# Optimization experiments

Measured on AMD Instinct MI355X. Metric: run time of the kernel, lower is better.

## Reference

```python
import jax, jax.numpy as jnp
import numpy as np

B, C, N, T = 16, 32, 1024, 64
C_OUT = 32
ORDER = 2
SMOOTH_DEPTH = 1


def setup_inputs() -> dict:
    key = jax.random.key(0)
    k1, k2, k3, k4 = jax.random.split(key, 4)
    x = jax.random.normal(k1, (B, C, N, T), dtype=jnp.float32)
    # row-normalized dense adjacencies (transition matrices), as used in Graph-WaveNet-style supports
    AL = jax.random.uniform(k2, (N, N), dtype=jnp.float32)
    AL = AL / AL.sum(axis=-1, keepdims=True)
    AS_pos = jax.random.uniform(k3, (N, N), dtype=jnp.float32)
    AS_pos = AS_pos / AS_pos.sum(axis=-1, keepdims=True)
    # 1x1 conv mlp: in_channels = (order*support_len+1)*c_in = 3*C, out_channels = C_OUT
    W_mlp = jax.random.normal(k4, (C_OUT, (ORDER + 1) * C), dtype=jnp.float32) * 0.02
    b_mlp = jnp.zeros((C_OUT,), dtype=jnp.float32)
    return {"x": x, "AL": AL, "AS_pos": AS_pos, "W_mlp": W_mlp, "b_mlp": b_mlp}


def reference(x, AL, AS_pos, W_mlp, b_mlp):
    # gcn_module.forward with short_bool=True, smooth_depth=SMOOTH_DEPTH, eval mode (no dropout)
    ALp = jnp.linalg.matrix_power(AL, SMOOTH_DEPTH)          # [N,N]
    # torch.einsum('bckj,ik->bcij', x, ALp): contract node dim of x against ALp
    x_long = jnp.einsum('ik,bckt->bcit', ALp, x)             # [B,C,N,T]
    x_short = x - x_long
    outs = [x]
    for _ in range(ORDER):
        # dnconv: einsum('nvw,ncwl->ncvl', A, x) with 2D A broadcast over batch
        x_long = jnp.einsum('vw,bcwt->bcvt', AL, x_long)
        x_short = jnp.einsum('vw,bcwt->bcvt', AS_pos, x_short)
        outs.append(x_long + x_short)
    h = jnp.concatenate(outs, axis=1)                        # [B,(ORDER+1)*C,N,T]
    # 1x1 conv == channel mixing
    h = jnp.einsum('oc,bcnt->bont', W_mlp, h) + b_mlp[None, :, None, None]
    return h
```

## Files before the change

### kernel.cpp

```cpp
#include <hip/hip_runtime.h>


typedef __bf16 bf16x8 __attribute__((ext_vector_type(8)));
typedef float f32x4 __attribute__((ext_vector_type(4)));
typedef unsigned int u32x4 __attribute__((ext_vector_type(4)));
typedef unsigned int u32x2 __attribute__((ext_vector_type(2)));

__device__ __forceinline__ unsigned short f2bf(float f) {
  unsigned u = __builtin_bit_cast(unsigned, f);
  u += 0x7fffu + ((u >> 16) & 1u);
  return (unsigned short)(u >> 16);
}
__device__ __forceinline__ float bf2f(unsigned short h) {
  unsigned u = ((unsigned)h) << 16;
  return __builtin_bit_cast(float, u);
}

static constexpr size_t OFF_XT    = 0;
static constexpr size_t OFF_U     = 67108864;
static constexpr size_t OFF_ALBF  = 201326592;
static constexpr size_t OFF_ALT   = OFF_ALBF  + 2097152;
static constexpr size_t OFF_ASBF  = OFF_ALT   + 2097152;
static constexpr size_t OFF_AST   = OFF_ASBF  + 2097152;
static constexpr size_t OFF_AL2   = OFF_AST   + 2097152;
static constexpr size_t OFF_AL2T  = OFF_AL2   + 2097152;
static constexpr size_t OFF_ASAL  = OFF_AL2T  + 2097152;
static constexpr size_t OFF_AS2   = OFF_ASAL  + 2097152;
static constexpr size_t OFF_AL3   = OFF_AS2   + 2097152;
static constexpr size_t OFF_AS2AL = OFF_AL3   + 2097152;
static constexpr size_t OFF_G     = OFF_AS2AL + 2097152;

__global__ __launch_bounds__(256) void k_cast_bf16(const float* __restrict__ src,
                                                   unsigned short* __restrict__ dst,
                                                   int n4) {
  int i = blockIdx.x * 256 + threadIdx.x;
  if (i < n4) {
    float4 v = *((const float4*)src + i);
    unsigned lo = (unsigned)f2bf(v.x) | ((unsigned)f2bf(v.y) << 16);
    unsigned hi = (unsigned)f2bf(v.z) | ((unsigned)f2bf(v.w) << 16);
    u32x2 pk = {lo, hi};
    *(u32x2*)(dst + (size_t)i * 4) = pk;
  }
}

__global__ __launch_bounds__(256) void k_transpose_cast(const float* __restrict__ src,
                                                        unsigned short* __restrict__ dst,
                                                        int R, int Cc) {
  __shared__ float Xs[64][65];
  const int tid = threadIdx.x;
  const size_t slice = (size_t)blockIdx.z * (size_t)R * (size_t)Cc;
  const float* s = src + slice;
  unsigned short* d = dst + slice;
  const int r0 = blockIdx.x * 64, c0 = blockIdx.y * 64;
  const int lrow = tid >> 4, lc4 = tid & 15;
#pragma unroll
  for (int rr = 0; rr < 4; rr++) {
    int row = rr * 16 + lrow;
    float4 v = *(const float4*)(s + (size_t)(r0 + row) * Cc + c0 + lc4 * 4);
    Xs[row][lc4 * 4 + 0] = v.x;
    Xs[row][lc4 * 4 + 1] = v.y;
    Xs[row][lc4 * 4 + 2] = v.z;
    Xs[row][lc4 * 4 + 3] = v.w;
  }
  __syncthreads();
  const int wc = tid & 7;
#pragma unroll
  for (int u = 0; u < 2; u++) {
    int t = u * 32 + (tid >> 3);
    unsigned v0 = (unsigned)f2bf(Xs[wc * 8 + 0][t]) | ((unsigned)f2bf(Xs[wc * 8 + 1][t]) << 16);
    unsigned v1 = (unsigned)f2bf(Xs[wc * 8 + 2][t]) | ((unsigned)f2bf(Xs[wc * 8 + 3][t]) << 16);
    unsigned v2 = (unsigned)f2bf(Xs[wc * 8 + 4][t]) | ((unsigned)f2bf(Xs[wc * 8 + 5][t]) << 16);
    unsigned v3 = (unsigned)f2bf(Xs[wc * 8 + 6][t]) | ((unsigned)f2bf(Xs[wc * 8 + 7][t]) << 16);
    u32x4 pk = {v0, v1, v2, v3};
    *(u32x4*)(d + (size_t)(c0 + t) * R + r0 + wc * 8) = pk;
  }
}

__device__ __forceinline__ void gemm128_bt(const unsigned short* __restrict__ A,
                                           const unsigned short* __restrict__ Bt,
                                           unsigned short* __restrict__ Cp,
                                           int K, size_t ldc, int m0, int n0) {
  __shared__ unsigned short As[128 * 32];
  __shared__ unsigned short Bs[128 * 32];
  const int tid = threadIdx.x;
  const int wave = tid >> 6, lane = tid & 63;
  const int lane15 = lane & 15, quad = lane >> 4;
  const int wm = wave & 1, wn = wave >> 1;
  const int srow = lane >> 2;
  const int schunk = (lane & 3) * 8;

  const unsigned short* gA0 = A + (size_t)(m0 + wave * 16 + srow) * K + schunk;
  const unsigned short* gA1 = A + (size_t)(m0 + 64 + wave * 16 + srow) * K + schunk;
  const unsigned short* gB0 = Bt + (size_t)(n0 + wave * 16 + srow) * K + schunk;
  const unsigned short* gB1 = Bt + (size_t)(n0 + 64 + wave * 16 + srow) * K + schunk;
  unsigned short* lA0 = As + (wave * 16) * 32;
  unsigned short* lA1 = As + (64 + wave * 16) * 32;
  unsigned short* lB0 = Bs + (wave * 16) * 32;
  unsigned short* lB1 = Bs + (64 + wave * 16) * 32;

  f32x4 acc[4][4];
#pragma unroll
  for (int i = 0; i < 4; i++)
#pragma unroll
    for (int j = 0; j < 4; j++) acc[i][j] = (f32x4){0.f, 0.f, 0.f, 0.f};

  const unsigned short* pa = As + (wm * 64 + lane15) * 32 + quad * 8;
  const unsigned short* pb = Bs + (wn * 64 + lane15) * 32 + quad * 8;

  for (int kb = 0; kb < K; kb += 32) {
    __syncthreads();
    __builtin_amdgcn_global_load_lds(
        (const __attribute__((address_space(1))) unsigned int*)(gA0 + kb),
        (__attribute__((address_space(3))) unsigned int*)lA0, 16, 0, 0);
    __builtin_amdgcn_global_load_lds(
        (const __attribute__((address_space(1))) unsigned int*)(gA1 + kb),
        (__attribute__((address_space(3))) unsigned int*)lA1, 16, 0, 0);
    __builtin_amdgcn_global_load_lds(
        (const __attribute__((address_space(1))) unsigned int*)(gB0 + kb),
        (__attribute__((address_space(3))) unsigned int*)lB0, 16, 0, 0);
    __builtin_amdgcn_global_load_lds(
        (const __attribute__((address_space(1))) unsigned int*)(gB1 + kb),
        (__attribute__((address_space(3))) unsigned int*)lB1, 16, 0, 0);
    __syncthreads();

    bf16x8 av[4], bv[4];
#pragma unroll
    for (int mt = 0; mt < 4; mt++) av[mt] = *(const bf16x8*)(pa + mt * 16 * 32);
#pragma unroll
    for (int nt = 0; nt < 4; nt++) bv[nt] = *(const bf16x8*)(pb + nt * 16 * 32);
#pragma unroll
    for (int mt = 0; mt < 4; mt++)
#pragma unroll
      for (int nt = 0; nt < 4; nt++)
        acc[mt][nt] = __builtin_amdgcn_mfma_f32_16x16x32_bf16(av[mt], bv[nt], acc[mt][nt], 0, 0, 0);
  }

#pragma unroll
  for (int mt = 0; mt < 4; mt++) {
#pragma unroll
    for (int nt = 0; nt < 4; nt++) {
      const int col = n0 + wn * 64 + nt * 16 + lane15;
#pragma unroll
      for (int r = 0; r < 4; r++) {
        const int row = m0 + wm * 64 + mt * 16 + quad * 4 + r;
        Cp[(size_t)row * ldc + col] = f2bf(acc[mt][nt][r]);
      }
    }
  }
}

__global__ __launch_bounds__(256) void k_gemm_pre(char* ws, int stage) {
  const unsigned short* A;
  const unsigned short* Bt;
  unsigned short* Cp;
  const int z = blockIdx.z;
  unsigned short* ALbf = (unsigned short*)(ws + OFF_ALBF);
  unsigned short* ALt  = (unsigned short*)(ws + OFF_ALT);
  unsigned short* ASbf = (unsigned short*)(ws + OFF_ASBF);
  unsigned short* ASt  = (unsigned short*)(ws + OFF_AST);
  unsigned short* AL2  = (unsigned short*)(ws + OFF_AL2);
  unsigned short* AL2t = (unsigned short*)(ws + OFF_AL2T);
  unsigned short* ASAL = (unsigned short*)(ws + OFF_ASAL);
  unsigned short* AS2  = (unsigned short*)(ws + OFF_AS2);
  unsigned short* AL3  = (unsigned short*)(ws + OFF_AL3);
  unsigned short* AS2AL= (unsigned short*)(ws + OFF_AS2AL);
  if (stage == 0) {
    if (z == 0)      { A = ALbf; Bt = ALt;  Cp = AL2;  }
    else if (z == 1) { A = ALt;  Bt = ALbf; Cp = AL2t; }
    else if (z == 2) { A = ASbf; Bt = ALt;  Cp = ASAL; }
    else             { A = ASbf; Bt = ASt;  Cp = AS2;  }
  } else {
    if (z == 0)      { A = ALbf; Bt = AL2t; Cp = AL3;  }
    else             { A = AS2;  Bt = ALt;  Cp = AS2AL;}
  }
  gemm128_bt(A, Bt, Cp, 1024, 1024, blockIdx.y * 128, blockIdx.x * 128);
}

__global__ __launch_bounds__(256) void k_assemble_G(const unsigned short* __restrict__ AL2,
                                                    const unsigned short* __restrict__ ASAL,
                                                    const float* __restrict__ ASf,
                                                    const unsigned short* __restrict__ AL3,
                                                    const unsigned short* __restrict__ AS2,
                                                    const unsigned short* __restrict__ AS2AL,
                                                    unsigned short* __restrict__ G) {
  int i = blockIdx.x * 256 + threadIdx.x;
  float g1 = bf2f(AL2[i]) + ASf[i] - bf2f(ASAL[i]);
  G[i] = f2bf(g1);
  float g2 = bf2f(AL3[i]) + bf2f(AS2[i]) - bf2f(AS2AL[i]);
  G[1048576 + i] = f2bf(g2);
}

__global__ __launch_bounds__(256) void k_gemm_main(const unsigned short* __restrict__ G,
                                                   const unsigned short* __restrict__ xT,
                                                   unsigned short* __restrict__ U) {
  gemm128_bt(G, xT, U, 1024, 32768, blockIdx.y * 128, blockIdx.x * 128);
}

__device__ __forceinline__ int swz_off(int j, int kc) {
  int s = (j ^ (j >> 3) ^ (j >> 6)) & 7;
  return (kc ^ s) << 3;
}

__global__ __launch_bounds__(256) void k_mix_mfma(const float* __restrict__ x,
                                                  const unsigned short* __restrict__ U,
                                                  const unsigned short* __restrict__ Wbf,
                                                  const float* __restrict__ bm,
                                                  float* __restrict__ out) {
  __shared__ unsigned short Hs[128 * 128];
  const int tid = threadIdx.x;
  const int b  = blockIdx.x >> 9;
  const int n0 = (blockIdx.x & 511) * 2;

  const float* xb = x + (size_t)b * 2097152 + (size_t)n0 * 64;
#pragma unroll
  for (int i = 0; i < 4; i++) {
    int q = tid + 256 * i;
    int p = q >> 4;
    int c = p >> 1, nn = p & 1;
    int t0 = (q & 15) * 4;
    float4 v = *(const float4*)(xb + (size_t)c * 65536 + nn * 64 + t0);
    int kc = c >> 3, wi = c & 7;
    float vv[4] = {v.x, v.y, v.z, v.w};
#pragma unroll
    for (int e = 0; e < 4; e++) {
      int j = nn * 64 + t0 + e;
      Hs[j * 128 + swz_off(j, kc) + wi] = f2bf(vv[e]);
    }
  }
#pragma unroll
  for (int i = 0; i < 4; i++) {
    int q = tid + 256 * i;
    int row = q >> 8;
    int g = row >> 1, nn = row & 1;
    int s8 = (q & 255) * 8;
    int c = s8 >> 6, t0 = s8 & 63;
    const unsigned short* src =
        U + (size_t)(g * 1024 + n0 + nn) * 32768 + (size_t)b * 2048 + s8;
    u32x4 v = *(const u32x4*)src;
    int kc = 4 + g * 4 + (c >> 3), wi = c & 7;
#pragma unroll
    for (int e = 0; e < 4; e++) {
      int j0 = nn * 64 + t0 + 2 * e;
      unsigned w = v[e];
      Hs[j0 * 128 + swz_off(j0, kc) + wi]       = (unsigned short)(w & 0xffffu);
      Hs[(j0 + 1) * 128 + swz_off(j0 + 1, kc) + wi] = (unsigned short)(w >> 16);
    }
  }
  __syncthreads();

  const int wave = tid >> 6, lane = tid & 63;
  const int lane15 = lane & 15, quad = lane >> 4;
  f32x4 acc[2][2];
#pragma unroll
  for (int jt = 0; jt < 2; jt++)
#pragma unroll
    for (int ot = 0; ot < 2; ot++) acc[jt][ot] = (f32x4){0.f, 0.f, 0.f, 0.f};

#pragma unroll
  for (int kchunk = 0; kchunk < 3; kchunk++) {
    bf16x8 bv[2];
#pragma unroll
    for (int ot = 0; ot < 2; ot++)
      bv[ot] = *(const bf16x8*)(Wbf + (ot * 16 + lane15) * 96 + kchunk * 32 + quad * 8);
#pragma unroll
    for (int jt = 0; jt < 2; jt++) {
      int j = wave * 32 + jt * 16 + lane15;
      bf16x8 av = *(const bf16x8*)(Hs + j * 128 + swz_off(j, kchunk * 4 + quad));
#pragma unroll
      for (int ot = 0; ot < 2; ot++)
        acc[jt][ot] = __builtin_amdgcn_mfma_f32_16x16x32_bf16(av, bv[ot], acc[jt][ot], 0, 0, 0);
    }
  }

#pragma unroll
  for (int jt = 0; jt < 2; jt++) {
#pragma unroll
    for (int ot = 0; ot < 2; ot++) {
      int col = ot * 16 + lane15;
      float bo = bm[col];
#pragma unroll
      for (int r = 0; r < 4; r++) {
        int j = wave * 32 + jt * 16 + quad * 4 + r;
        int nn = j >> 6, t = j & 63;
        out[(size_t)b * 2097152 + (size_t)col * 65536 + (size_t)(n0 + nn) * 64 + t] =
            acc[jt][ot][r] + bo;
      }
    }
  }
}

extern "C" void kernel_launch(void* const* d_in, const int* in_sizes, int n_in,
                              void* d_out, int out_size, void* d_ws, size_t ws_size,
                              hipStream_t stream) {
  const float* x  = (const float*)d_in[0];
  const float* AL = (const float*)d_in[1];
  const float* AS = (const float*)d_in[2];
  const float* W  = (const float*)d_in[3];
  const float* bm = (const float*)d_in[4];
  float* out = (float*)d_out;
  char* ws = (char*)d_ws;

  unsigned short* xT    = (unsigned short*)(ws + OFF_XT);
  unsigned short* U     = (unsigned short*)(ws + OFF_U);
  unsigned short* ALbf  = (unsigned short*)(ws + OFF_ALBF);
  unsigned short* ALt   = (unsigned short*)(ws + OFF_ALT);
  unsigned short* ASbf  = (unsigned short*)(ws + OFF_ASBF);
  unsigned short* ASt   = (unsigned short*)(ws + OFF_AST);
  unsigned short* AL2   = (unsigned short*)(ws + OFF_AL2);
  unsigned short* ASAL  = (unsigned short*)(ws + OFF_ASAL);
  unsigned short* AS2   = (unsigned short*)(ws + OFF_AS2);
  unsigned short* AL3   = (unsigned short*)(ws + OFF_AL3);
  unsigned short* AS2AL = (unsigned short*)(ws + OFF_AS2AL);
  unsigned short* Gm    = (unsigned short*)(ws + OFF_G);
  unsigned short* Wbf   = (unsigned short*)(ws + OFF_ALBF);

  k_cast_bf16<<<1024, 256, 0, stream>>>(AL, ALbf, 262144);
  k_cast_bf16<<<1024, 256, 0, stream>>>(AS, ASbf, 262144);
  k_transpose_cast<<<dim3(16, 16, 1), 256, 0, stream>>>(AL, ALt, 1024, 1024);
  k_transpose_cast<<<dim3(16, 16, 1), 256, 0, stream>>>(AS, ASt, 1024, 1024);
  k_transpose_cast<<<dim3(16, 1, 512), 256, 0, stream>>>(x, xT, 1024, 64);
  k_gemm_pre<<<dim3(8, 8, 4), 256, 0, stream>>>(ws, 0);
  k_gemm_pre<<<dim3(8, 8, 2), 256, 0, stream>>>(ws, 1);
  k_assemble_G<<<4096, 256, 0, stream>>>(AL2, ASAL, AS, AL3, AS2, AS2AL, Gm);
  k_cast_bf16<<<3, 256, 0, stream>>>(W, Wbf, 768);
  k_gemm_main<<<dim3(256, 16, 1), 256, 0, stream>>>(Gm, xT, U);
  k_mix_mfma<<<dim3(8192, 1, 1), 256, 0, stream>>>(x, U, Wbf, bm, out);
}
```

Baseline: 521.8 us.

## Replace main GEMM with 256x256-tile, 8-wave kernel using async LDS double buffering

```diff
diff --git a/kernel.cpp b/kernel.cpp
--- a/kernel.cpp
+++ b/kernel.cpp
@@ -190,10 +190,216 @@
   G[1048576 + i] = f2bf(g2);
 }
 
-__global__ __launch_bounds__(256) void k_gemm_main(const unsigned short* __restrict__ G,
-                                                   const unsigned short* __restrict__ xT,
-                                                   unsigned short* __restrict__ U) {
-  gemm128_bt(G, xT, U, 1024, 32768, blockIdx.y * 128, blockIdx.x * 128);
+__global__ __launch_bounds__(512) void k_gemm_main8(const unsigned short* __restrict__ A,
+                                                    const unsigned short* __restrict__ Bt,
+                                                    unsigned short* __restrict__ C) {
+  __shared__ unsigned short lds[65536];
+  const int tid = threadIdx.x;
+  const int wave = tid >> 6, lane = tid & 63;
+  const int lane15 = lane & 15, quad = lane >> 4;
+  const int wr = wave >> 2, wc = wave & 3;
+
+  const int bid = blockIdx.x;
+  const int swz = (bid & 7) * 128 + (bid >> 3);
+  const int nx = swz >> 3, my = swz & 7;
+  const int m0 = my * 256, n0 = nx * 256;
+
+  const int srow = tid >> 3;
+  const int skc  = (((tid & 7) ^ (srow & 7)) << 3);
+  const int ldst0 = (tid & ~63) << 3;
+
+#define STAGE_HALF(gbase, rowbase, ldsptr, ktile)                                       \
+  do {                                                                                  \
+    const unsigned short* _g =                                                          \
+        (gbase) + (size_t)((rowbase) + srow) * 1024 + (size_t)((ktile) * 64 + skc);     \
+    __builtin_amdgcn_global_load_lds(                                                   \
+        (const __attribute__((address_space(1))) unsigned int*)_g,                      \
+        (__attribute__((address_space(3))) unsigned int*)((ldsptr) + ldst0), 16, 0, 0); \
+    __builtin_amdgcn_global_load_lds(                                                   \
+        (const __attribute__((address_space(1))) unsigned int*)(_g + 65536),            \
+        (__attribute__((address_space(3))) unsigned int*)((ldsptr) + 4096 + ldst0),     \
+        16, 0, 0);                                                                      \
+  } while (0)
+
+#define LOAD_AFR(p)                                                                     \
+  bf16x8 afr[2][2];                                                                     \
+  _Pragma("unroll") for (int mi = 0; mi < 2; mi++)                                      \
+      _Pragma("unroll") for (int kk = 0; kk < 2; kk++)                                  \
+          afr[mi][kk] = *(const bf16x8*)(pA + (2 * (p) + mi) * 1024 + aks[kk]);
+
+#define MFMA_QUAD(p)                                                                    \
+  _Pragma("unroll") for (int kk = 0; kk < 2; kk++)                                      \
+      _Pragma("unroll") for (int mi = 0; mi < 2; mi++)                                  \
+          _Pragma("unroll") for (int n = 0; n < 4; n++)                                 \
+              acc[2 * (p) + mi][n] = __builtin_amdgcn_mfma_f32_16x16x32_bf16(           \
+                  afr[mi][kk], bfr[n][kk], acc[2 * (p) + mi][n], 0, 0, 0);
+
+#define PHASE_SYNC_PRE()                              \
+  asm volatile("" ::: "memory");                      \
+  __builtin_amdgcn_s_barrier();                       \
+  asm volatile("s_waitcnt lgkmcnt(0)" ::: "memory");  \
+  __builtin_amdgcn_sched_barrier(0);                  \
+  __builtin_amdgcn_s_setprio(1);
+
+#define PHASE_SYNC_POST()                             \
+  __builtin_amdgcn_s_setprio(0);                      \
+  asm volatile("" ::: "memory");                      \
+  __builtin_amdgcn_s_barrier();
+
+  unsigned short* Acur = lds;
+  unsigned short* Bcur = lds + 16384;
+  unsigned short* Aalt = lds + 32768;
+  unsigned short* Balt = lds + 49152;
+
+  f32x4 acc[8][4];
+#pragma unroll
+  for (int i = 0; i < 8; i++)
+#pragma unroll
+    for (int j = 0; j < 4; j++) acc[i][j] = (f32x4){0.f, 0.f, 0.f, 0.f};
+
+  const int swz8 = (lane15 & 7) << 3;
+  int aks[2];
+  aks[0] = (quad << 3) ^ swz8;
+  aks[1] = (32 | (quad << 3)) ^ swz8;
+
+  STAGE_HALF(Bt, n0,       Bcur,        0);
+  STAGE_HALF(Bt, n0 + 128, Bcur + 8192, 0);
+  STAGE_HALF(A,  m0,       Acur,        0);
+  STAGE_HALF(A,  m0 + 128, Acur + 8192, 0);
+  STAGE_HALF(Bt, n0,       Balt,        1);
+  STAGE_HALF(Bt, n0 + 128, Balt + 8192, 1);
+  STAGE_HALF(A,  m0,       Aalt,        1);
+  asm volatile("s_waitcnt vmcnt(6)" ::: "memory");
+  __builtin_amdgcn_s_barrier();
+
+  for (int u = 0; u < 14; ++u) {
+    const unsigned short* pA = Acur + (wr * 128 + lane15) * 64;
+    const unsigned short* pB = Bcur + (wc * 64 + lane15) * 64;
+    bf16x8 bfr[4][2];
+    {
+#pragma unroll
+      for (int n = 0; n < 4; n++)
+#pragma unroll
+        for (int kk = 0; kk < 2; kk++)
+          bfr[n][kk] = *(const bf16x8*)(pB + n * 1024 + aks[kk]);
+      LOAD_AFR(0)
+      __builtin_amdgcn_sched_barrier(0);
+      STAGE_HALF(A, m0 + 128, Aalt + 8192, u + 1);
+      asm volatile("s_waitcnt lgkmcnt(8)" ::: "memory");
+      PHASE_SYNC_PRE()
+      MFMA_QUAD(0)
+      PHASE_SYNC_POST()
+    }
+    {
+      LOAD_AFR(1)
+      __builtin_amdgcn_sched_barrier(0);
+      STAGE_HALF(Bt, n0, Bcur, u + 2);
+      PHASE_SYNC_PRE()
+      MFMA_QUAD(1)
+      PHASE_SYNC_POST()
+    }
+    {
+      LOAD_AFR(2)
+      __builtin_amdgcn_sched_barrier(0);
+      STAGE_HALF(Bt, n0 + 128, Bcur + 8192, u + 2);
+      PHASE_SYNC_PRE()
+      MFMA_QUAD(2)
+      PHASE_SYNC_POST()
+    }
+    {
+      LOAD_AFR(3)
+      __builtin_amdgcn_sched_barrier(0);
+      STAGE_HALF(A, m0, Acur, u + 2);
+      PHASE_SYNC_PRE()
+      MFMA_QUAD(3)
+      __builtin_amdgcn_s_setprio(0);
+      asm volatile("s_waitcnt vmcnt(6)" ::: "memory");
+      asm volatile("" ::: "memory");
+      __builtin_amdgcn_s_barrier();
+    }
+    unsigned short* t;
+    t = Acur; Acur = Aalt; Aalt = t;
+    t = Bcur; Bcur = Balt; Balt = t;
+  }
+
+  {
+    const unsigned short* pA = Acur + (wr * 128 + lane15) * 64;
+    const unsigned short* pB = Bcur + (wc * 64 + lane15) * 64;
+    bf16x8 bfr[4][2];
+    {
+#pragma unroll
+      for (int n = 0; n < 4; n++)
+#pragma unroll
+        for (int kk = 0; kk < 2; kk++)
+          bfr[n][kk] = *(const bf16x8*)(pB + n * 1024 + aks[kk]);
+      LOAD_AFR(0)
+      __builtin_amdgcn_sched_barrier(0);
+      STAGE_HALF(A, m0 + 128, Aalt + 8192, 15);
+      asm volatile("s_waitcnt lgkmcnt(8)" ::: "memory");
+      PHASE_SYNC_PRE()
+      MFMA_QUAD(0)
+      PHASE_SYNC_POST()
+    }
+    { LOAD_AFR(1) PHASE_SYNC_PRE() MFMA_QUAD(1) PHASE_SYNC_POST() }
+    { LOAD_AFR(2) PHASE_SYNC_PRE() MFMA_QUAD(2) PHASE_SYNC_POST() }
+    {
+      LOAD_AFR(3)
+      PHASE_SYNC_PRE()
+      MFMA_QUAD(3)
+      __builtin_amdgcn_s_setprio(0);
+      asm volatile("s_waitcnt vmcnt(0)" ::: "memory");
+      asm volatile("" ::: "memory");
+      __builtin_amdgcn_s_barrier();
+    }
+    unsigned short* t;
+    t = Acur; Acur = Aalt; Aalt = t;
+    t = Bcur; Bcur = Balt; Balt = t;
+  }
+
+  {
+    const unsigned short* pA = Acur + (wr * 128 + lane15) * 64;
+    const unsigned short* pB = Bcur + (wc * 64 + lane15) * 64;
+    bf16x8 bfr[4][2];
+#pragma unroll
+    for (int n = 0; n < 4; n++)
+#pragma unroll
+      for (int kk = 0; kk < 2; kk++)
+        bfr[n][kk] = *(const bf16x8*)(pB + n * 1024 + aks[kk]);
+#pragma unroll
+    for (int p = 0; p < 4; p++) {
+      bf16x8 afr[2][2];
+#pragma unroll
+      for (int mi = 0; mi < 2; mi++)
+#pragma unroll
+        for (int kk = 0; kk < 2; kk++)
+          afr[mi][kk] = *(const bf16x8*)(pA + (2 * p + mi) * 1024 + aks[kk]);
+#pragma unroll
+      for (int kk = 0; kk < 2; kk++)
+#pragma unroll
+        for (int mi = 0; mi < 2; mi++)
+#pragma unroll
+          for (int n = 0; n < 4; n++)
+            acc[2 * p + mi][n] = __builtin_amdgcn_mfma_f32_16x16x32_bf16(
+                afr[mi][kk], bfr[n][kk], acc[2 * p + mi][n], 0, 0, 0);
+    }
+  }
+
+#pragma unroll
+  for (int mt = 0; mt < 8; mt++) {
+    const int row = m0 + wr * 128 + mt * 16 + quad * 4;
+#pragma unroll
+    for (int n = 0; n < 4; n++) {
+      const int col = n0 + wc * 64 + n * 16 + lane15;
+#pragma unroll
+      for (int r = 0; r < 4; r++)
+        C[(size_t)(row + r) * 32768 + col] = f2bf(acc[mt][n][r]);
+    }
+  }
+#undef STAGE_HALF
+#undef LOAD_AFR
+#undef MFMA_QUAD
+#undef PHASE_SYNC_PRE
+#undef PHASE_SYNC_POST
 }
 
 __device__ __forceinline__ int swz_off(int j, int kc) {
@@ -233,16 +439,16 @@
     int row = q >> 8;
     int g = row >> 1, nn = row & 1;
     int s8 = (q & 255) * 8;
-    int c = s8 >> 6, t0 = s8 & 63;
+    int c = s8 >> 6;
     const unsigned short* src =
         U + (size_t)(g * 1024 + n0 + nn) * 32768 + (size_t)b * 2048 + s8;
     u32x4 v = *(const u32x4*)src;
     int kc = 4 + g * 4 + (c >> 3), wi = c & 7;
 #pragma unroll
     for (int e = 0; e < 4; e++) {
-      int j0 = nn * 64 + t0 + 2 * e;
+      int j0 = nn * 64 + (s8 & 63) + 2 * e;
       unsigned w = v[e];
-      Hs[j0 * 128 + swz_off(j0, kc) + wi]       = (unsigned short)(w & 0xffffu);
+      Hs[j0 * 128 + swz_off(j0, kc) + wi]           = (unsigned short)(w & 0xffffu);
       Hs[(j0 + 1) * 128 + swz_off(j0 + 1, kc) + wi] = (unsigned short)(w >> 16);
     }
   }
@@ -323,6 +529,6 @@
   k_gemm_pre<<<dim3(8, 8, 2), 256, 0, stream>>>(ws, 1);
   k_assemble_G<<<4096, 256, 0, stream>>>(AL2, ASAL, AS, AL3, AS2, AS2AL, Gm);
   k_cast_bf16<<<3, 256, 0, stream>>>(W, Wbf, 768);
-  k_gemm_main<<<dim3(256, 16, 1), 256, 0, stream>>>(Gm, xT, U);
+  k_gemm_main8<<<dim3(1024, 1, 1), 512, 0, stream>>>(Gm, xT, U);
   k_mix_mfma<<<dim3(8192, 1, 1), 256, 0, stream>>>(x, U, Wbf, bm, out);
 }
```

Result: faster. 497.4 us (-4.7%).
